# Performance work log

Hardware: AMD Instinct MI355X
Metric: run time of the kernel (lower is better)

Reference implementation:

```python
import jax, jax.numpy as jnp
import numpy as np

B = 100          # batch_size -> dist matrix is [2B, 2B]
G = 2            # pairs
REG = 0.1
H = W = 256
EPS = 1e-08


def computemask(b, g):
    # Faithful numpy port of the torch computemask (pure python, constants).
    Mask, labels = [], []
    mtxsize = 2 * b
    for j in range(mtxsize):
        i = j
        x = [i - i % g - i // b * b,
             i + 1 - i % g - i // b * b,
             i - i % g - i // b * b + b,
             i + 1 - i % g - i // b * b + b]
        x.remove(j)
        for xi in x:
            xx = x.copy()
            indexs = list(range(mtxsize))
            indexs.remove(j)
            xx.remove(xi)
            for r in xx:
                indexs.remove(r)
            labels.append(indexs.index(xi))
            Mask.append(indexs)
    return np.asarray(Mask, np.int32), np.asarray(labels, np.int32)


def setup_inputs() -> dict:
    key = jax.random.key(0)
    x = jax.random.normal(key, (2 * B, 1, H, W), dtype=jnp.float32)
    m, l = computemask(B, G)              # [6B, 2B-3], [6B]
    return {"x": x, "masks": jnp.asarray(m), "labels": jnp.asarray(l)}


def _euclidean_distance_matrix(x):
    xf = x.reshape(x.shape[0], -1)                      # [N, H*W]
    dot = xf @ xf.T                                     # [N, N] Gram GEMM
    sq = jnp.diagonal(dot)
    d = sq[None, :] - 2.0 * dot + sq[:, None]
    d = jnp.maximum(d, 0.0)
    mask = (d == 0.0).astype(x.dtype)
    d = jnp.sqrt(d + mask * EPS) * (1.0 - mask)
    return d


def _calc_psd(xs):
    dft = jnp.fft.fft2(xs)                              # [N, H, W] complex
    avgpsd = jnp.mean((dft * jnp.conj(dft)).real, axis=0)  # [H, W]
    return jnp.mean(jnp.log(avgpsd)) - jnp.log(jnp.mean(avgpsd))


def reference(x, masks, labels):
    xs = jnp.squeeze(x)                                 # [2B, H, W]
    dist = _euclidean_distance_matrix(xs)               # [2B, 2B]
    # create_pairs: logits[m] = dist[m // 3][masks[m]]  -> [6B, 2B-3]
    rows = jnp.arange(masks.shape[0]) // 3
    logits = dist[rows[:, None], masks]
    logp = jax.nn.log_softmax(logits, axis=-1)
    ce = -jnp.mean(logp[jnp.arange(labels.shape[0]), labels])
    return ce - REG * _calc_psd(xs)
```

## Files before the change

### kernel.cpp

```cpp
#include <hip/hip_runtime.h>
#include <hip/hip_bf16.h>
#include <math.h>


#define NIMG 200
#define NROW 256
#define NCOL 256
#define NPIX 65536
#define TSTR 132
#define ISTR 264
#define XSTR 273
#define NCH  50
#define IPC  4
#define GNK  64
#define GKC  1024
#define CLDS 17472

typedef float2 c2;
typedef short bf16x8 __attribute__((ext_vector_type(8)));
typedef unsigned short u16x8 __attribute__((ext_vector_type(8)));
typedef float f32x4  __attribute__((ext_vector_type(4)));

#define BAR_LDS() do {                                            \
    __builtin_amdgcn_sched_barrier(0);                            \
    asm volatile("s_waitcnt lgkmcnt(0)" ::: "memory");            \
    __builtin_amdgcn_s_barrier();                                 \
    __builtin_amdgcn_sched_barrier(0);                            \
} while (0)

__device__ __forceinline__ unsigned short f2b(float f) {
    union { float f; unsigned int u; } c; c.f = f;
    unsigned int r = (c.u + 0x7FFFu + ((c.u >> 16) & 1u)) >> 16;
    return (unsigned short)r;
}
__device__ __forceinline__ float b2f(unsigned short b) {
    union { unsigned int u; float f; } c; c.u = ((unsigned int)b) << 16;
    return c.f;
}

__device__ __forceinline__ c2 cmul(c2 a, c2 b) {
    return make_float2(a.x*b.x - a.y*b.y, a.x*b.y + a.y*b.x);
}
__device__ __forceinline__ c2 cadd(c2 a, c2 b){ return make_float2(a.x+b.x, a.y+b.y); }
__device__ __forceinline__ c2 csub(c2 a, c2 b){ return make_float2(a.x-b.x, a.y-b.y); }
__device__ __forceinline__ c2 mulmi(c2 a){ return make_float2(a.y, -a.x); }

__device__ __forceinline__ void fft4(c2& a, c2& b, c2& c, c2& d) {
    c2 t0 = cadd(a,c), t1 = csub(a,c), t2 = cadd(b,d), t3 = csub(b,d);
    a = cadd(t0,t2);
    c = csub(t0,t2);
    c2 mt3 = mulmi(t3);
    b = cadd(t1, mt3);
    d = csub(t1, mt3);
}

__device__ __forceinline__ void fft16(c2 x[16]) {
    #pragma unroll
    for (int j=0;j<4;j++) fft4(x[j], x[4+j], x[8+j], x[12+j]);
    const c2 W1 = make_float2( 0.9238795325112867f,-0.3826834323650898f);
    const c2 W2 = make_float2( 0.7071067811865476f,-0.7071067811865476f);
    const c2 W3 = make_float2( 0.3826834323650898f,-0.9238795325112867f);
    const c2 W6 = make_float2(-0.7071067811865476f,-0.7071067811865476f);
    const c2 W9 = make_float2(-0.9238795325112867f, 0.3826834323650898f);
    x[5]=cmul(x[5],W1);   x[6]=cmul(x[6],W2);   x[7]=cmul(x[7],W3);
    x[9]=cmul(x[9],W2);   x[10]=mulmi(x[10]);   x[11]=cmul(x[11],W6);
    x[13]=cmul(x[13],W3); x[14]=cmul(x[14],W6); x[15]=cmul(x[15],W9);
    #pragma unroll
    for (int k1=0;k1<4;k1++) fft4(x[4*k1], x[4*k1+1], x[4*k1+2], x[4*k1+3]);
}
#define R4(q) ((((q)&3)<<2)|((q)>>2))

__global__ __launch_bounds__(512) void k_gc(const unsigned short* __restrict__ Xb,
                                            float* __restrict__ Pg,
                                            const ushort2* __restrict__ T,
                                            float* __restrict__ Ppart) {
    __shared__ __align__(16) char smem[2*CLDS];
    int bid = blockIdx.x;
    int tid = threadIdx.x;

    if (bid < 192) {
        unsigned short* As = (unsigned short*)smem;
        unsigned short* Bs = (unsigned short*)(smem + 16384);
        int p  = bid >> 6;
        int kc = bid & 63;
        int ti = p >> 1, tj = (p + 1) >> 1;
        bool diag = (ti == tj);
        int i0 = ti << 7, j0 = tj << 7;
        int wid = tid >> 6, lane = tid & 63;
        int wr = wid >> 2, wc = wid & 3;

        f32x4 acc[4][2];
        #pragma unroll
        for (int a=0;a<4;a++)
            #pragma unroll
            for (int b=0;b<2;b++) acc[a][b] = (f32x4){0.f,0.f,0.f,0.f};

        int srow = tid >> 2, g0 = (tid & 3) * 2;
        int gia = i0 + srow; if (gia > 199) gia = 199;
        int gjb = j0 + srow; if (gjb > 199) gjb = 199;
        const u16x8* Ap = (const u16x8*)(Xb + ((size_t)kc*200 + gia)*GKC);
        const u16x8* Bp = (const u16x8*)(Xb + ((size_t)kc*200 + gjb)*GKC);
        int e0 = (srow*128 + g0*16) ^ ((srow & 7) << 4);
        int e1 = (srow*128 + (g0+1)*16) ^ ((srow & 7) << 4);

        int swz = (lane & 7) << 3;
        int acol0 = (lane >> 4) << 3;

        u16x8 ca0 = Ap[g0], ca1 = Ap[g0+1];
        u16x8 cb0, cb1;
        if (!diag) { cb0 = Bp[g0]; cb1 = Bp[g0+1]; }

        #pragma unroll 1
        for (int st = 0; st < GKC/64; ++st) {
            BAR_LDS();
            *(u16x8*)((char*)As + e0) = ca0;
            *(u16x8*)((char*)As + e1) = ca1;
            if (!diag) {
                *(u16x8*)((char*)Bs + e0) = cb0;
                *(u16x8*)((char*)Bs + e1) = cb1;
            }
            if (st < GKC/64 - 1) {
                ca0 = Ap[(st+1)*8 + g0]; ca1 = Ap[(st+1)*8 + g0+1];
                if (!diag) { cb0 = Bp[(st+1)*8 + g0]; cb1 = Bp[(st+1)*8 + g0+1]; }
            }
            BAR_LDS();
            const unsigned short* Bb = diag ? As : Bs;
            #pragma unroll
            for (int ks=0; ks<2; ++ks) {
                int col = (ks*32 + acol0) ^ swz;
                bf16x8 af[4], bfv[2];
                #pragma unroll
                for (int mf=0; mf<4; ++mf) {
                    int r = wr*64 + mf*16 + (lane & 15);
                    af[mf] = *(const bf16x8*)(&As[r*64 + col]);
                }
                #pragma unroll
                for (int nf=0; nf<2; ++nf) {
                    int r = wc*32 + nf*16 + (lane & 15);
                    bfv[nf] = *(const bf16x8*)(&Bb[r*64 + col]);
                }
                #pragma unroll
                for (int mf=0; mf<4; ++mf)
                    #pragma unroll
                    for (int nf=0; nf<2; ++nf)
                        acc[mf][nf] = __builtin_amdgcn_mfma_f32_16x16x32_bf16(af[mf], bfv[nf], acc[mf][nf], 0, 0, 0);
            }
        }
        float* P = Pg + ((size_t)p*GNK + kc)*16384;
        #pragma unroll
        for (int mf=0; mf<4; ++mf) {
            int m0 = wr*64 + mf*16 + ((lane >> 4) << 2);
            #pragma unroll
            for (int nf=0; nf<2; ++nf) {
                int n = wc*32 + nf*16 + (lane & 15);
                #pragma unroll
                for (int r2=0; r2<4; ++r2)
                    P[(size_t)(m0+r2)*128 + n] = acc[mf][nf][r2];
            }
        }
    } else {
        int team = tid >> 8;
        int t256 = tid & 255;
        ushort2* sb = (ushort2*)(smem + team*CLDS);
        int gteam = (bid - 192)*2 + team;
        int cgi = gteam % 9, ic = gteam / 9;
        int c0 = cgi * 16;
        int g = t256 >> 4, t = t256 & 15;
        int cc = t256 & 15, rb = t256 >> 4;
        int cl = c0 + cc; if (cl > 128) cl = 128;
        c2 Wb;
        {
            float sv, cv;
            sincosf(-0.024543692606170259f * (float)t, &sv, &cv);
            Wb = make_float2(cv, sv);
        }
        float pacc[16];
        #pragma unroll
        for (int q=0;q<16;q++) pacc[q] = 0.f;

        for (int li=0; li<IPC; ++li) {
            int img = ic*IPC + li;
            __syncthreads();
            const ushort2* Tb = T + (size_t)img*NROW*TSTR;
            #pragma unroll
            for (int j=0;j<16;j++) {
                int r = rb*16 + j;
                sb[cc*XSTR + r] = Tb[(size_t)r*TSTR + cl];
            }
            __syncthreads();
            c2 y[16];
            #pragma unroll
            for (int n1=0;n1<16;n1++) {
                ushort2 u = sb[g*XSTR + 16*n1 + t];
                y[n1] = make_float2(b2f(u.x), b2f(u.y));
            }
            fft16(y);
            {
                c2 cur = Wb;
                #pragma unroll
                for (int r=1;r<16;r++) { y[R4(r)] = cmul(y[R4(r)], cur); cur = cmul(cur, Wb); }
            }
            __syncthreads();
            #pragma unroll
            for (int r=0;r<16;r++) {
                c2 v = y[R4(r)];
                sb[g*XSTR + t*17 + r] = make_ushort2(f2b(v.x), f2b(v.y));
            }
            __syncthreads();
            c2 w[16];
            #pragma unroll
            for (int n2=0;n2<16;n2++) {
                ushort2 u = sb[g*XSTR + n2*17 + t];
                w[n2] = make_float2(b2f(u.x), b2f(u.y));
            }
            fft16(w);
            #pragma unroll
            for (int q=0;q<16;q++) { c2 v = w[R4(q)]; pacc[q] += v.x*v.x + v.y*v.y; }
        }
        int c = c0 + g;
        if (c <= 128) {
            float* PP = Ppart + ((size_t)ic*132 + c)*256;
            #pragma unroll
            for (int q=0;q<16;q++) PP[q*16 + t] = pacc[q];
        }
    }
}

__global__ __launch_bounds__(256) void k_gredu(const float* __restrict__ Pg,
                                               float* __restrict__ dotm) {
    int idx = blockIdx.x*256 + threadIdx.x;
    if (idx >= 200*200) return;
    int i = idx / 200, j = idx - i*200;
    int ti = i >> 7, tj = j >> 7;
    int p, li, lj;
    if (ti <= tj) { p = ti + tj; li = i - (ti << 7); lj = j - (tj << 7); }
    else          { p = 1;       li = j;             lj = i - 128; }
    const float* base = Pg + (size_t)p*GNK*16384 + (size_t)li*128 + lj;
    float s0=0.f, s1=0.f, s2=0.f, s3=0.f;
    #pragma unroll 4
    for (int kc=0; kc<GNK; kc+=4) {
        s0 += base[(size_t)(kc  )*16384];
        s1 += base[(size_t)(kc+1)*16384];
        s2 += base[(size_t)(kc+2)*16384];
        s3 += base[(size_t)(kc+3)*16384];
    }
    dotm[(size_t)i*200 + j] = (s0+s1) + (s2+s3);
}

__global__ __launch_bounds__(256) void k_rowfft(const float* __restrict__ x,
                                                ushort2* __restrict__ T,
                                                unsigned short* __restrict__ Xb) {
    __shared__ __align__(16) char ldsraw[16*XSTR*4];
    float*   inpF = (float*)ldsraw;
    ushort2* tb   = (ushort2*)ldsraw;
    int tid = threadIdx.x;
    int img = blockIdx.y;
    int rg  = blockIdx.x;
    int g = tid >> 4, t = tid & 15;
    int row = rg*16 + g;

    const float4* xr = (const float4*)(x + (size_t)img*NPIX + (size_t)row*NCOL + t*16);
    float4 v0 = xr[0], v1 = xr[1], v2 = xr[2], v3 = xr[3];
    u16x8 h0, h1;
    h0[0]=f2b(v0.x); h0[1]=f2b(v0.y); h0[2]=f2b(v0.z); h0[3]=f2b(v0.w);
    h0[4]=f2b(v1.x); h0[5]=f2b(v1.y); h0[6]=f2b(v1.z); h0[7]=f2b(v1.w);
    h1[0]=f2b(v2.x); h1[1]=f2b(v2.y); h1[2]=f2b(v2.z); h1[3]=f2b(v2.w);
    h1[4]=f2b(v3.x); h1[5]=f2b(v3.y); h1[6]=f2b(v3.z); h1[7]=f2b(v3.w);
    {
        unsigned short* Xo = Xb + (((size_t)(row >> 2)*NIMG + img)*GKC
                                   + (size_t)(row & 3)*256 + t*16);
        *(u16x8*)(Xo)     = h0;
        *(u16x8*)(Xo + 8) = h1;
    }
    float* ip = inpF + g*ISTR + t*16;
    *(float4*)(ip)    = v0;
    *(float4*)(ip+4)  = v1;
    *(float4*)(ip+8)  = v2;
    *(float4*)(ip+12) = v3;
    __syncthreads();

    c2 y[16];
    #pragma unroll
    for (int n1=0;n1<16;n1++) y[n1] = make_float2(inpF[g*ISTR + 16*n1 + t], 0.f);
    fft16(y);
    {
        float sv, cv;
        sincosf(-0.024543692606170259f * (float)t, &sv, &cv);
        c2 Wb = make_float2(cv, sv);
        c2 cur = Wb;
        #pragma unroll
        for (int r=1;r<16;r++) { y[R4(r)] = cmul(y[R4(r)], cur); cur = cmul(cur, Wb); }
    }
    __syncthreads();
    #pragma unroll
    for (int r=0;r<16;r++) {
        c2 v = y[R4(r)];
        tb[g*XSTR + t*17 + r] = make_ushort2(f2b(v.x), f2b(v.y));
    }
    __syncthreads();

    c2 w[16];
    #pragma unroll
    for (int n2=0;n2<16;n2++) {
        ushort2 u = tb[g*XSTR + n2*17 + t];
        w[n2] = make_float2(b2f(u.x), b2f(u.y));
    }
    fft16(w);
    ushort2* To = T + ((size_t)img*NROW + row)*TSTR;
    #pragma unroll
    for (int q=0;q<8;q++) {
        c2 v = w[R4(q)];
        To[q*16 + t] = make_ushort2(f2b(v.x), f2b(v.y));
    }
    if (t == 0) { c2 v = w[R4(8)]; To[128] = make_ushort2(f2b(v.x), f2b(v.y)); }
}

__global__ __launch_bounds__(256) void k_tail(const float* __restrict__ Ppart,
                                              const float* __restrict__ dotm,
                                              const int* __restrict__ masks,
                                              const int* __restrict__ labels,
                                              float* __restrict__ cep,
                                              float2* __restrict__ Pred) {
    int bid = blockIdx.x, tid = threadIdx.x;
    if (bid < 129) {
        int c = bid;
        float s = 0.f;
        for (int ic=0; ic<NCH; ++ic) s += Ppart[((size_t)ic*132 + c)*256 + tid];
        float v = s * (1.0f/200.0f);
        float w = (c == 0 || c == 128) ? 1.f : 2.f;
        float sl = w * logf(v);
        float ss = w * v;
        __shared__ float r2[2][4];
        int wv = tid>>6, ln = tid&63;
        #pragma unroll
        for (int off=32; off>=1; off>>=1) {
            sl += __shfl_xor(sl, off);
            ss += __shfl_xor(ss, off);
        }
        if (ln == 0) { r2[0][wv] = sl; r2[1][wv] = ss; }
        __syncthreads();
        if (tid == 0)
            Pred[c] = make_float2(r2[0][0]+r2[0][1]+r2[0][2]+r2[0][3],
                                  r2[1][0]+r2[1][1]+r2[1][2]+r2[1][3]);
    } else {
        int m = (bid - 129)*4 + (tid >> 6);
        if (m >= 600) return;
        int lane = tid & 63;
        int i = m / 3;
        float sqi = dotm[(size_t)i*200 + i];
        int lbl = labels[m];
        float lg[4];
        float vmax = -1e30f, lsel = 0.f;
        #pragma unroll
        for (int k=0;k<4;k++) {
            int c = lane + 64*k;
            float v = -1e30f;
            if (c < 197) {
                int j = masks[(size_t)m*197 + c];
                float d = sqi + dotm[(size_t)j*200 + j] - 2.f*dotm[(size_t)i*200 + j];
                d = fmaxf(d, 0.f);
                v = (d == 0.f) ? 0.f : sqrtf(d);
                if (c == lbl) lsel = v;
            }
            lg[k] = v;
            vmax = fmaxf(vmax, v);
        }
        #pragma unroll
        for (int off=32; off>=1; off>>=1) vmax = fmaxf(vmax, __shfl_xor(vmax, off));
        float se = 0.f;
        #pragma unroll
        for (int k=0;k<4;k++) if (lg[k] > -1e29f) se += expf(lg[k] - vmax);
        #pragma unroll
        for (int off=32; off>=1; off>>=1) { se += __shfl_xor(se, off); lsel += __shfl_xor(lsel, off); }
        if (lane == 0) cep[m] = lsel - (vmax + logf(se));
    }
}

__global__ __launch_bounds__(256) void k_final(const float2* __restrict__ Pred,
                                               const float* __restrict__ cep,
                                               float* __restrict__ out) {
    int tid = threadIdx.x;
    float sl = 0.f, ss = 0.f, sce = 0.f;
    if (tid < 129) { float2 p = Pred[tid]; sl = p.x; ss = p.y; }
    for (int m = tid; m < 600; m += 256) sce += cep[m];
    __shared__ float r3[3][4];
    int wv = tid>>6, ln = tid&63;
    #pragma unroll
    for (int off=32; off>=1; off>>=1) {
        sl  += __shfl_xor(sl, off);
        ss  += __shfl_xor(ss, off);
        sce += __shfl_xor(sce, off);
    }
    if (ln == 0) { r3[0][wv]=sl; r3[1][wv]=ss; r3[2][wv]=sce; }
    __syncthreads();
    if (tid == 0) {
        float SL = r3[0][0]+r3[0][1]+r3[0][2]+r3[0][3];
        float SS = r3[1][0]+r3[1][1]+r3[1][2]+r3[1][3];
        float CE = r3[2][0]+r3[2][1]+r3[2][2]+r3[2][3];
        float ce  = -CE / 600.f;
        float psd = SL * (1.f/65536.f) - logf(SS * (1.f/65536.f));
        out[0] = ce - 0.1f * psd;
    }
}

extern "C" void kernel_launch(void* const* d_in, const int* in_sizes, int n_in,
                              void* d_out, int out_size, void* d_ws, size_t ws_size,
                              hipStream_t stream) {
    const float* x      = (const float*)d_in[0];
    const int*   masks  = (const int*)d_in[1];
    const int*   labels = (const int*)d_in[2];
    float* out = (float*)d_out;
    char* ws = (char*)d_ws;

    const size_t OFF_DOT = 0;
    const size_t OFF_CE  = 160256;
    const size_t OFF_PR  = 162688;
    const size_t OFF_PP  = 163840;
    const size_t OFF_T   = 6922240;
    const size_t OFF_XB  = 33955840;
    const size_t OFF_PG  = 60170240;
    const size_t NEED    = 72753152;
    if (ws_size < NEED) return;

    float*          dotm = (float*)(ws + OFF_DOT);
    float*          cep  = (float*)(ws + OFF_CE);
    float2*         Pr   = (float2*)(ws + OFF_PR);
    float*          Pp   = (float*)(ws + OFF_PP);
    ushort2*        T    = (ushort2*)(ws + OFF_T);
    unsigned short* Xb   = (unsigned short*)(ws + OFF_XB);
    float*          Pg   = (float*)(ws + OFF_PG);

    k_rowfft<<<dim3(16,200), dim3(256), 0, stream>>>(x, T, Xb);
    k_gc    <<<dim3(417),    dim3(512), 0, stream>>>(Xb, Pg, T, Pp);
    k_gredu <<<dim3(157),    dim3(256), 0, stream>>>(Pg, dotm);
    k_tail  <<<dim3(279),    dim3(256), 0, stream>>>(Pp, dotm, masks, labels, cep, Pr);
    k_final <<<dim3(1),      dim3(256), 0, stream>>>(Pr, cep, out);
}
```

Before: 73.46 us.

## Store row-FFT intermediate column-major so column FFT reads it with vector loads

The row-FFT kernel now transposes its 16-row tile through shared memory and writes the intermediate spectrum in a column-major layout (column, row) with 16-byte vector stores. The column-FFT stage can then read each column's 16 rows as four contiguous vector loads instead of sixteen strided 4-byte gathers. This adds an extra LDS transpose and barrier in the row kernel, and only 129 of 256 threads take part in the global store.

```diff
diff --git a/kernel.cpp b/kernel.cpp
--- a/kernel.cpp
+++ b/kernel.cpp
@@ -7,9 +7,9 @@
 #define NROW 256
 #define NCOL 256
 #define NPIX 65536
-#define TSTR 132
 #define ISTR 264
 #define XSTR 273
+#define TCS  20
 #define NCH  50
 #define IPC  4
 #define GNK  64
@@ -181,12 +181,17 @@
         for (int li=0; li<IPC; ++li) {
             int img = ic*IPC + li;
             __syncthreads();
-            const ushort2* Tb = T + (size_t)img*NROW*TSTR;
-            #pragma unroll
-            for (int j=0;j<16;j++) {
-                int r = rb*16 + j;
-                sb[cc*XSTR + r] = Tb[(size_t)r*TSTR + cl];
-            }
+            const u16x8* src = (const u16x8*)(T + ((size_t)img*132 + cl)*256 + rb*16);
+            u16x8 v0 = src[0], v1 = src[1], v2 = src[2], v3 = src[3];
+            ushort2* dstl = sb + cc*XSTR + rb*16;
+            #pragma unroll
+            for (int j=0;j<4;j++) dstl[j]    = ((const ushort2*)&v0)[j];
+            #pragma unroll
+            for (int j=0;j<4;j++) dstl[4+j]  = ((const ushort2*)&v1)[j];
+            #pragma unroll
+            for (int j=0;j<4;j++) dstl[8+j]  = ((const ushort2*)&v2)[j];
+            #pragma unroll
+            for (int j=0;j<4;j++) dstl[12+j] = ((const ushort2*)&v3)[j];
             __syncthreads();
             c2 y[16];
             #pragma unroll
@@ -253,6 +258,7 @@
     __shared__ __align__(16) char ldsraw[16*XSTR*4];
     float*   inpF = (float*)ldsraw;
     ushort2* tb   = (ushort2*)ldsraw;
+    ushort2* tc   = (ushort2*)ldsraw;
     int tid = threadIdx.x;
     int img = blockIdx.y;
     int rg  = blockIdx.x;
@@ -305,14 +311,24 @@
         ushort2 u = tb[g*XSTR + n2*17 + t];
         w[n2] = make_float2(b2f(u.x), b2f(u.y));
     }
+    __syncthreads();
     fft16(w);
-    ushort2* To = T + ((size_t)img*NROW + row)*TSTR;
     #pragma unroll
     for (int q=0;q<8;q++) {
         c2 v = w[R4(q)];
-        To[q*16 + t] = make_ushort2(f2b(v.x), f2b(v.y));
-    }
-    if (t == 0) { c2 v = w[R4(8)]; To[128] = make_ushort2(f2b(v.x), f2b(v.y)); }
+        tc[(q*16 + t)*TCS + g] = make_ushort2(f2b(v.x), f2b(v.y));
+    }
+    if (t == 0) {
+        c2 v = w[R4(8)];
+        tc[128*TCS + g] = make_ushort2(f2b(v.x), f2b(v.y));
+    }
+    __syncthreads();
+    if (tid < 129) {
+        const u16x8* src = (const u16x8*)(tc + (size_t)tid*TCS);
+        u16x8 a = src[0], b = src[1], c = src[2], d = src[3];
+        u16x8* dst = (u16x8*)(T + ((size_t)img*132 + tid)*256 + rg*16);
+        dst[0] = a; dst[1] = b; dst[2] = c; dst[3] = d;
+    }
 }
 
 __global__ __launch_bounds__(256) void k_tail(const float* __restrict__ Ppart,
```

Measured after the change: 75.52 us. +2.8%, slower.

## Shrink fused GEMM/FFT blocks to 256 threads with larger per-wave tiles

Applied to the files above, without the earlier changes.

The fused Gram-GEMM/column-FFT kernel drops from 512 to 256 threads per block. In the GEMM branch each of the 4 waves now computes a 64x64 sub-tile (4x4 MFMA fragments), and each thread stages four 16-byte chunks per operand. In the FFT branch each block now holds a single team instead of two, so the grid grows from 417 to 642 blocks. The goal is smaller blocks that schedule more flexibly and more register-level reuse of operands per MFMA, at the cost of more accumulator registers per thread and fewer waves to hide latency within each GEMM block.

```diff
diff --git a/kernel.cpp b/kernel.cpp
--- a/kernel.cpp
+++ b/kernel.cpp
@@ -14,7 +14,6 @@
 #define IPC  4
 #define GNK  64
 #define GKC  1024
-#define CLDS 17472
 
 typedef float2 c2;
 typedef short bf16x8 __attribute__((ext_vector_type(8)));
@@ -70,11 +69,11 @@
 }
 #define R4(q) ((((q)&3)<<2)|((q)>>2))
 
-__global__ __launch_bounds__(512) void k_gc(const unsigned short* __restrict__ Xb,
+__global__ __launch_bounds__(256) void k_gc(const unsigned short* __restrict__ Xb,
                                             float* __restrict__ Pg,
                                             const ushort2* __restrict__ T,
                                             float* __restrict__ Ppart) {
-    __shared__ __align__(16) char smem[2*CLDS];
+    __shared__ __align__(16) char smem[32768];
     int bid = blockIdx.x;
     int tid = threadIdx.x;
 
@@ -87,62 +86,69 @@
         bool diag = (ti == tj);
         int i0 = ti << 7, j0 = tj << 7;
         int wid = tid >> 6, lane = tid & 63;
-        int wr = wid >> 2, wc = wid & 3;
-
-        f32x4 acc[4][2];
+        int wr = wid >> 1, wc = wid & 1;
+
+        f32x4 acc[4][4];
         #pragma unroll
         for (int a=0;a<4;a++)
             #pragma unroll
-            for (int b=0;b<2;b++) acc[a][b] = (f32x4){0.f,0.f,0.f,0.f};
-
-        int srow = tid >> 2, g0 = (tid & 3) * 2;
+            for (int b=0;b<4;b++) acc[a][b] = (f32x4){0.f,0.f,0.f,0.f};
+
+        int srow = tid >> 1, gq = (tid & 1) * 4;
         int gia = i0 + srow; if (gia > 199) gia = 199;
         int gjb = j0 + srow; if (gjb > 199) gjb = 199;
         const u16x8* Ap = (const u16x8*)(Xb + ((size_t)kc*200 + gia)*GKC);
         const u16x8* Bp = (const u16x8*)(Xb + ((size_t)kc*200 + gjb)*GKC);
-        int e0 = (srow*128 + g0*16) ^ ((srow & 7) << 4);
-        int e1 = (srow*128 + (g0+1)*16) ^ ((srow & 7) << 4);
+        int e0 = (srow*128 + (gq  )*16) ^ ((srow & 7) << 4);
+        int e1 = (srow*128 + (gq+1)*16) ^ ((srow & 7) << 4);
+        int e2 = (srow*128 + (gq+2)*16) ^ ((srow & 7) << 4);
+        int e3 = (srow*128 + (gq+3)*16) ^ ((srow & 7) << 4);
 
         int swz = (lane & 7) << 3;
         int acol0 = (lane >> 4) << 3;
 
-        u16x8 ca0 = Ap[g0], ca1 = Ap[g0+1];
-        u16x8 cb0, cb1;
-        if (!diag) { cb0 = Bp[g0]; cb1 = Bp[g0+1]; }
+        u16x8 a0 = Ap[gq], a1 = Ap[gq+1], a2 = Ap[gq+2], a3 = Ap[gq+3];
+        u16x8 b0, b1, b2, b3;
+        if (!diag) { b0 = Bp[gq]; b1 = Bp[gq+1]; b2 = Bp[gq+2]; b3 = Bp[gq+3]; }
 
         #pragma unroll 1
         for (int st = 0; st < GKC/64; ++st) {
             BAR_LDS();
-            *(u16x8*)((char*)As + e0) = ca0;
-            *(u16x8*)((char*)As + e1) = ca1;
+            *(u16x8*)((char*)As + e0) = a0;
+            *(u16x8*)((char*)As + e1) = a1;
+            *(u16x8*)((char*)As + e2) = a2;
+            *(u16x8*)((char*)As + e3) = a3;
             if (!diag) {
-                *(u16x8*)((char*)Bs + e0) = cb0;
-                *(u16x8*)((char*)Bs + e1) = cb1;
+                *(u16x8*)((char*)Bs + e0) = b0;
+                *(u16x8*)((char*)Bs + e1) = b1;
+                *(u16x8*)((char*)Bs + e2) = b2;
+                *(u16x8*)((char*)Bs + e3) = b3;
             }
             if (st < GKC/64 - 1) {
-                ca0 = Ap[(st+1)*8 + g0]; ca1 = Ap[(st+1)*8 + g0+1];
-                if (!diag) { cb0 = Bp[(st+1)*8 + g0]; cb1 = Bp[(st+1)*8 + g0+1]; }
+                int b = (st+1)*8 + gq;
+                a0 = Ap[b]; a1 = Ap[b+1]; a2 = Ap[b+2]; a3 = Ap[b+3];
+                if (!diag) { b0 = Bp[b]; b1 = Bp[b+1]; b2 = Bp[b+2]; b3 = Bp[b+3]; }
             }
             BAR_LDS();
             const unsigned short* Bb = diag ? As : Bs;
             #pragma unroll
             for (int ks=0; ks<2; ++ks) {
                 int col = (ks*32 + acol0) ^ swz;
-                bf16x8 af[4], bfv[2];
+                bf16x8 af[4], bfv[4];
                 #pragma unroll
                 for (int mf=0; mf<4; ++mf) {
                     int r = wr*64 + mf*16 + (lane & 15);
                     af[mf] = *(const bf16x8*)(&As[r*64 + col]);
                 }
                 #pragma unroll
-                for (int nf=0; nf<2; ++nf) {
-                    int r = wc*32 + nf*16 + (lane & 15);
+                for (int nf=0; nf<4; ++nf) {
+                    int r = wc*64 + nf*16 + (lane & 15);
                     bfv[nf] = *(const bf16x8*)(&Bb[r*64 + col]);
                 }
                 #pragma unroll
                 for (int mf=0; mf<4; ++mf)
                     #pragma unroll
-                    for (int nf=0; nf<2; ++nf)
+                    for (int nf=0; nf<4; ++nf)
                         acc[mf][nf] = __builtin_amdgcn_mfma_f32_16x16x32_bf16(af[mf], bfv[nf], acc[mf][nf], 0, 0, 0);
             }
         }
@@ -151,22 +157,20 @@
         for (int mf=0; mf<4; ++mf) {
             int m0 = wr*64 + mf*16 + ((lane >> 4) << 2);
             #pragma unroll
-            for (int nf=0; nf<2; ++nf) {
-                int n = wc*32 + nf*16 + (lane & 15);
+            for (int nf=0; nf<4; ++nf) {
+                int n = wc*64 + nf*16 + (lane & 15);
                 #pragma unroll
                 for (int r2=0; r2<4; ++r2)
                     P[(size_t)(m0+r2)*128 + n] = acc[mf][nf][r2];
             }
         }
     } else {
-        int team = tid >> 8;
-        int t256 = tid & 255;
-        ushort2* sb = (ushort2*)(smem + team*CLDS);
-        int gteam = (bid - 192)*2 + team;
+        ushort2* sb = (ushort2*)smem;
+        int gteam = bid - 192;
         int cgi = gteam % 9, ic = gteam / 9;
         int c0 = cgi * 16;
-        int g = t256 >> 4, t = t256 & 15;
-        int cc = t256 & 15, rb = t256 >> 4;
+        int g = tid >> 4, t = tid & 15;
+        int cc = tid & 15, rb = tid >> 4;
         int cl = c0 + cc; if (cl > 128) cl = 128;
         c2 Wb;
         {
@@ -431,7 +435,7 @@
     float*          Pg   = (float*)(ws + OFF_PG);
 
     k_rowfft<<<dim3(16,200), dim3(256), 0, stream>>>(x, T, Xb);
-    k_gc    <<<dim3(417),    dim3(512), 0, stream>>>(Xb, Pg, T, Pp);
+    k_gc    <<<dim3(642),    dim3(256), 0, stream>>>(Xb, Pg, T, Pp);
     k_gredu <<<dim3(157),    dim3(256), 0, stream>>>(Pg, dotm);
     k_tail  <<<dim3(279),    dim3(256), 0, stream>>>(Pp, dotm, masks, labels, cep, Pr);
     k_final <<<dim3(1),      dim3(256), 0, stream>>>(Pr, cep, out);
```

New measurement: 72.49 us. Within noise of the previous version (-1.3%).
